# Kernel tuning notes

Hardware: AMD Instinct MI355X
Metric: run time of the kernel (lower is better)

Reference implementation:

```python
import jax, jax.numpy as jnp
import numpy as np
from jax import lax


def setup_inputs() -> dict:
    key = jax.random.key(0)
    k1, k2, k3 = jax.random.split(key, 3)
    x = jax.random.normal(k1, (16, 32, 48, 48, 48), dtype=jnp.float32)
    w = jax.random.normal(k2, (64, 32, 3, 3, 3), dtype=jnp.float32) * 0.05
    b = jax.random.normal(k3, (64,), dtype=jnp.float32) * 0.05
    return {"x": x, "w": w, "b": b}


def reference(x, w, b):
    # conv3d, stride=1, padding=1 (NCDHW / OIDHW)
    y = lax.conv_general_dilated(
        x, w,
        window_strides=(1, 1, 1),
        padding=[(1, 1), (1, 1), (1, 1)],
        dimension_numbers=("NCDHW", "OIDHW", "NCDHW"),
    )
    y = y + b[None, :, None, None, None]  # [N, Cout, 48, 48, 48]
    # maxpool3d kernel=2 stride=2 (ceil_mode=False)
    y = lax.reduce_window(
        y, -jnp.inf, lax.max,
        window_dimensions=(1, 1, 2, 2, 2),
        window_strides=(1, 1, 2, 2, 2),
        padding="VALID",
    )  # [N, Cout, 24, 24, 24]
    # logsumexp over channel dim (keepdim), then ReLU
    lse = jax.nn.logsumexp(y, axis=1, keepdims=True)  # [N, 1, 24, 24, 24]
    return jnp.maximum(lse, 0.0)
```

## Files before the change

kernel.cpp:

```cpp
#include <hip/hip_runtime.h>
#include <math.h>

#define CIN 32
#define COUT 64
#define DIM 48
#define PD 24
#define D3 110592

#define XP_POS 125000
#define XB_BYTES 128000000ull

typedef __bf16 bf16x8 __attribute__((ext_vector_type(8)));
typedef __bf16 bf16x4 __attribute__((ext_vector_type(4)));
typedef float f32x4 __attribute__((ext_vector_type(4)));

__device__ __forceinline__ unsigned bf16_rne(float f) {
    unsigned u = __builtin_bit_cast(unsigned, f);
    return (u + 0x7fffu + ((u >> 16) & 1u)) >> 16;
}

__global__ __launch_bounds__(256) void wpack_kernel(const float* __restrict__ w,
                                                    unsigned short* __restrict__ wg) {
    int i = blockIdx.x * 256 + threadIdx.x;
    if (i >= 27 * 64 * 32) return;
    int cin = i & 31, cout = (i >> 5) & 63, tap = i >> 11;
    float v = w[(cout * CIN + cin) * 27 + tap];
    wg[i] = (unsigned short)bf16_rne(v);
}

__global__ __launch_bounds__(256) void xpack_kernel(const float* __restrict__ x,
                                                    unsigned short* __restrict__ xb) {
    int i = blockIdx.x * 256 + threadIdx.x;
    if (i >= 16 * XP_POS) return;
    int pw = i % 50, t = i / 50, ph = t % 50, t2 = t / 50, pd = t2 % 50, n = t2 / 50;
    uint4* dst = (uint4*)(xb + (size_t)i * 32);
    int gd = pd - 1, gh = ph - 1, gw = pw - 1;
    if ((unsigned)gd < 48u && (unsigned)gh < 48u && (unsigned)gw < 48u) {
        const float* p = x + (size_t)n * CIN * D3 + ((size_t)gd * DIM + gh) * DIM + gw;
        unsigned pk[16];
#pragma unroll
        for (int cp = 0; cp < 16; ++cp) {
            float a = p[(size_t)(2 * cp) * D3];
            float b = p[(size_t)(2 * cp + 1) * D3];
            pk[cp] = bf16_rne(a) | (bf16_rne(b) << 16);
        }
#pragma unroll
        for (int q = 0; q < 4; ++q)
            dst[q] = make_uint4(pk[4 * q], pk[4 * q + 1], pk[4 * q + 2], pk[4 * q + 3]);
    } else {
        uint4 z = make_uint4(0, 0, 0, 0);
#pragma unroll
        for (int q = 0; q < 4; ++q) dst[q] = z;
    }
}

__global__ __launch_bounds__(256, 2) void conv_mfma_kernel(
    const unsigned short* __restrict__ xb, const unsigned short* __restrict__ wg,
    const float* __restrict__ bias, float* __restrict__ out)
{
    __shared__ __align__(16) unsigned short xs[1080 * 36];

    const int tid = threadIdx.x;
    const int bw = blockIdx.x % 3;
    const int bh = (blockIdx.x / 3) % 12;
    const int bd = (blockIdx.x / 36) % 6;
    const int n  = blockIdx.x / 216;

    const unsigned short* xtile = xb + (size_t)n * (XP_POS * 32)
                                + (size_t)(bd * 8) * (2500 * 32)
                                + (bh * 4) * (50 * 32) + (bw * 16) * 32;

    uint4 stg[17];
#pragma unroll
    for (int it = 0; it < 17; ++it) {
        int q = tid + it * 256;
        if (q < 4320) {
            int row = q >> 2, c = q & 3;
            int lw = row % 18, t = row / 18, lh = t % 6, ld = t / 6;
            stg[it] = *(const uint4*)(xtile + (size_t)ld * 80000 + lh * 1600 + lw * 32 + c * 8);
        }
    }
#pragma unroll
    for (int it = 0; it < 17; ++it) {
        int q = tid + it * 256;
        if (q < 4320) {
            int row = q >> 2, c = q & 3;
            char* p = (char*)xs + row * 72 + c * 16;
            *(uint2*)p       = make_uint2(stg[it].x, stg[it].y);
            *(uint2*)(p + 8) = make_uint2(stg[it].z, stg[it].w);
        }
    }

    const int lane = tid & 63;
    const int wv = tid >> 6;
    const int m  = lane & 15;
    const int ch = lane >> 4;

    const unsigned short* wgp = wg + m * 32 + ch * 8;

    float breg[4];
#pragma unroll
    for (int nt = 0; nt < 4; ++nt) breg[nt] = bias[nt * 16 + m];

    bf16x8 bcur[4], bnxt[4];
#pragma unroll
    for (int nt = 0; nt < 4; ++nt)
        bcur[nt] = *(const bf16x8*)(wgp + nt * 512);

    __syncthreads();

    f32x4 acc[2][4][4];
#pragma unroll
    for (int j = 0; j < 2; ++j)
#pragma unroll
        for (int i = 0; i < 4; ++i)
#pragma unroll
            for (int k = 0; k < 4; ++k)
                acc[j][i][k] = (f32x4)0.f;

#pragma unroll
    for (int tap = 0; tap < 27; ++tap) {
        if (tap < 26) {
#pragma unroll
            for (int nt = 0; nt < 4; ++nt)
                bnxt[nt] = *(const bf16x8*)(wgp + (tap + 1) * 2048 + nt * 512);
        }
        const int kd = tap / 9, kh = (tap / 3) % 3, kw = tap % 3;
        bf16x8 af[2][4];
#pragma unroll
        for (int j = 0; j < 2; ++j)
#pragma unroll
            for (int hz = 0; hz < 4; ++hz) {
                const int row = ((2 * wv + j + kd) * 6 + (hz + kh)) * 18 + (m + kw);
                const unsigned short* p = xs + row * 36 + ch * 8;
                bf16x4 lo = *(const bf16x4*)p;
                bf16x4 hi = *(const bf16x4*)(p + 4);
                af[j][hz] = __builtin_shufflevector(lo, hi, 0, 1, 2, 3, 4, 5, 6, 7);
            }
#pragma unroll
        for (int j = 0; j < 2; ++j)
#pragma unroll
            for (int hz = 0; hz < 4; ++hz)
#pragma unroll
                for (int nt = 0; nt < 4; ++nt)
                    acc[j][hz][nt] = __builtin_amdgcn_mfma_f32_16x16x32_bf16(
                        af[j][hz], bcur[nt], acc[j][hz][nt], 0, 0, 0);
#pragma unroll
        for (int nt = 0; nt < 4; ++nt) bcur[nt] = bnxt[nt];
    }
    __syncthreads();

    float* pooled = (float*)xs;
#pragma unroll
    for (int ph = 0; ph < 2; ++ph)
#pragma unroll
        for (int b = 0; b < 2; ++b)
#pragma unroll
            for (int nt = 0; nt < 4; ++nt) {
                float v =          acc[0][2 * ph][nt][2 * b];
                v = fmaxf(v,       acc[0][2 * ph][nt][2 * b + 1]);
                v = fmaxf(v,       acc[0][2 * ph + 1][nt][2 * b]);
                v = fmaxf(v,       acc[0][2 * ph + 1][nt][2 * b + 1]);
                v = fmaxf(v,       acc[1][2 * ph][nt][2 * b]);
                v = fmaxf(v,       acc[1][2 * ph][nt][2 * b + 1]);
                v = fmaxf(v,       acc[1][2 * ph + 1][nt][2 * b]);
                v = fmaxf(v,       acc[1][2 * ph + 1][nt][2 * b + 1]);
                int cell = (wv * 2 + ph) * 8 + 2 * ch + b;
                pooled[cell * 65 + nt * 16 + m] = v + breg[nt];
            }
    __syncthreads();

    if (tid < 64) {
        float mx = -INFINITY;
        for (int c = 0; c < 64; ++c) mx = fmaxf(mx, pooled[tid * 65 + c]);
        float s = 0.f;
        for (int c = 0; c < 64; ++c) s += __expf(pooled[tid * 65 + c] - mx);
        float r = fmaxf(mx + __logf(s), 0.f);
        int od = bd * 4 + (tid >> 4), oh = bh * 2 + ((tid >> 3) & 1), ow = bw * 8 + (tid & 7);
        out[((size_t)(n * PD + od) * PD + oh) * PD + ow] = r;
    }
}

__global__ __launch_bounds__(256, 3) void conv_mfma_r3(
    const float* __restrict__ x, const unsigned short* __restrict__ wg,
    const float* __restrict__ bias, float* __restrict__ out)
{
    __shared__ __align__(16) unsigned short xsr[648 * 40];
    const int tid = threadIdx.x;
    const int bw = blockIdx.x % 3;
    const int bh = (blockIdx.x / 3) % 12;
    const int bd = (blockIdx.x / 36) % 12;
    const int n  = blockIdx.x / 432;
    const int d0 = bd * 4 - 1, h0 = bh * 4 - 1, w0 = bw * 16 - 1;
    const float* xn = x + (size_t)n * CIN * D3;
    {
        const int cp = tid >> 4, sl = tid & 15;
        const float* xp0 = xn + (size_t)(cp * 2) * D3;
        for (int itb = 0; itb < 6; ++itb) {
            float f0[8], f1[8];
            int sv[8];
#pragma unroll
            for (int u = 0; u < 8; ++u) {
                const int s = sl + ((itb * 8 + u) << 4);
                sv[u] = s; f0[u] = 0.f; f1[u] = 0.f;
                if (s < 648) {
                    const int lw = s % 18, t = s / 18, lh = t % 6, ld = t / 6;
                    const int gd = d0 + ld, gh = h0 + lh, gw = w0 + lw;
                    if ((unsigned)gd < 48u && (unsigned)gh < 48u && (unsigned)gw < 48u) {
                        const float* p = xp0 + (gd * DIM + gh) * DIM + gw;
                        f0[u] = p[0]; f1[u] = p[D3];
                    }
                }
            }
#pragma unroll
            for (int u = 0; u < 8; ++u)
                if (sv[u] < 648)
                    ((unsigned*)xsr)[sv[u] * 20 + cp] = bf16_rne(f0[u]) | (bf16_rne(f1[u]) << 16);
        }
    }
    const int lane = tid & 63;
    const int wv = tid >> 6;
    const int m  = lane & 15;
    const int ch = lane >> 4;
    const unsigned short* wgp = wg + m * 32 + ch * 8;
    bf16x8 bcur[4], bnxt[4];
#pragma unroll
    for (int nt = 0; nt < 4; ++nt) bcur[nt] = *(const bf16x8*)(wgp + nt * 512);
    __syncthreads();
    f32x4 acc[4][4];
#pragma unroll
    for (int i = 0; i < 4; ++i)
#pragma unroll
        for (int j = 0; j < 4; ++j) acc[i][j] = (f32x4)0.f;
#pragma unroll
    for (int tap = 0; tap < 27; ++tap) {
        if (tap < 26) {
#pragma unroll
            for (int nt = 0; nt < 4; ++nt)
                bnxt[nt] = *(const bf16x8*)(wgp + (tap + 1) * 2048 + nt * 512);
        }
        const int kd = tap / 9, kh = (tap / 3) % 3, kw = tap % 3;
        bf16x8 af[4];
#pragma unroll
        for (int hz = 0; hz < 4; ++hz) {
            const int row = ((wv + kd) * 6 + (hz + kh)) * 18 + (m + kw);
            af[hz] = *(const bf16x8*)(xsr + row * 40 + ch * 8);
        }
#pragma unroll
        for (int hz = 0; hz < 4; ++hz)
#pragma unroll
            for (int nt = 0; nt < 4; ++nt)
                acc[hz][nt] = __builtin_amdgcn_mfma_f32_16x16x32_bf16(af[hz], bcur[nt], acc[hz][nt], 0, 0, 0);
#pragma unroll
        for (int nt = 0; nt < 4; ++nt) bcur[nt] = bnxt[nt];
    }
    __syncthreads();
    float* pmax = (float*)xsr;
#pragma unroll
    for (int ph = 0; ph < 2; ++ph)
#pragma unroll
        for (int b = 0; b < 2; ++b)
#pragma unroll
            for (int nt = 0; nt < 4; ++nt) {
                float v = fmaxf(fmaxf(acc[2 * ph][nt][2 * b], acc[2 * ph][nt][2 * b + 1]),
                                fmaxf(acc[2 * ph + 1][nt][2 * b], acc[2 * ph + 1][nt][2 * b + 1]));
                int pw = 2 * ch + b;
                pmax[((wv * 2 + ph) * 8 + pw) * 64 + nt * 16 + m] = v;
            }
    __syncthreads();
    float* pooled = pmax + 4096;
    for (int v = tid; v < 2048; v += 256) {
        int c = v & 63, cell = v >> 6;
        int pd = cell >> 4, ph = (cell >> 3) & 1, pw = cell & 7;
        int i1 = ((4 * pd + ph) * 8 + pw) * 64 + c;
        pooled[cell * 65 + c] = fmaxf(pmax[i1], pmax[i1 + 1024]) + bias[c];
    }
    __syncthreads();
    if (tid < 32) {
        int pd = tid >> 4, ph = (tid >> 3) & 1, pw = tid & 7;
        float mx = -INFINITY;
        for (int c = 0; c < 64; ++c) mx = fmaxf(mx, pooled[tid * 65 + c]);
        float s = 0.f;
        for (int c = 0; c < 64; ++c) s += __expf(pooled[tid * 65 + c] - mx);
        float r = fmaxf(mx + __logf(s), 0.f);
        int od = bd * 2 + pd, oh = bh * 2 + ph, ow = bw * 8 + pw;
        out[((size_t)(n * PD + od) * PD + oh) * PD + ow] = r;
    }
}

__global__ __launch_bounds__(256) void conv_fused_fallback(
    const float* __restrict__ x, const float* __restrict__ wsrc,
    const float* __restrict__ bias, float* __restrict__ out)
{
    __shared__ float smem[CIN * 216];
    const int tid = threadIdx.x;
    const int bid = blockIdx.x;
    const int tw = bid % 12, th = (bid / 12) % 12, td = (bid / 144) % 12, n = bid / 1728;
    const int d0 = td * 4, h0 = th * 4, w0 = tw * 4;
    const float* xn = x + (size_t)n * CIN * D3;
    for (int i = tid; i < CIN * 216; i += 256) {
        int cin = i / 216, r = i % 216;
        int dz = r / 36, hz = (r / 6) % 6, wz = r % 6;
        int gd = d0 - 1 + dz, gh = h0 - 1 + hz, gw = w0 - 1 + wz;
        float v = 0.f;
        if ((unsigned)gd < 48u && (unsigned)gh < 48u && (unsigned)gw < 48u)
            v = xn[((cin * DIM + gd) * DIM + gh) * DIM + gw];
        smem[i] = v;
    }
    __syncthreads();
    const int lane = tid & 63;
    const int wv = __builtin_amdgcn_readfirstlane(tid >> 6);
    const int cout0 = wv * 16;
    const int ld = lane >> 4, lh = (lane >> 2) & 3, lw = lane & 3;
    float acc[16];
#pragma unroll
    for (int c = 0; c < 16; ++c) acc[c] = 0.f;
    for (int cin = 0; cin < CIN; ++cin) {
        const int xb2 = cin * 216 + ld * 36 + lh * 6 + lw;
#pragma unroll
        for (int kd = 0; kd < 3; ++kd)
#pragma unroll
            for (int kh = 0; kh < 3; ++kh)
#pragma unroll
                for (int kw = 0; kw < 3; ++kw) {
                    const float xv = smem[xb2 + kd * 36 + kh * 6 + kw];
                    const int tap = (kd * 3 + kh) * 3 + kw;
#pragma unroll
                    for (int c = 0; c < 16; ++c)
                        acc[c] = fmaf(xv, wsrc[((cout0 + c) * CIN + cin) * 27 + tap], acc[c]);
                }
    }
    __syncthreads();
    float* cb = smem;
#pragma unroll
    for (int c = 0; c < 16; ++c) cb[(wv * 64 + lane) * 16 + c] = acc[c];
    __syncthreads();
    float* pool = smem + 4096;
    for (int v = tid; v < 512; v += 256) {
        const int pp = v >> 6, c = v & 63;
        const int pd = pp >> 2, ph = (pp >> 1) & 1, pw = pp & 1;
        float mv = -INFINITY;
#pragma unroll
        for (int i = 0; i < 2; ++i)
#pragma unroll
            for (int j = 0; j < 2; ++j)
#pragma unroll
                for (int k = 0; k < 2; ++k) {
                    const int l = ((2 * pd + i) << 4) | ((2 * ph + j) << 2) | (2 * pw + k);
                    mv = fmaxf(mv, cb[((c >> 4) * 64 + l) * 16 + (c & 15)]);
                }
        pool[pp * 64 + c] = mv + bias[c];
    }
    __syncthreads();
    if (tid < 8) {
        float mx = -INFINITY;
        for (int c = 0; c < 64; ++c) mx = fmaxf(mx, pool[tid * 64 + c]);
        float s = 0.f;
        for (int c = 0; c < 64; ++c) s += __expf(pool[tid * 64 + c] - mx);
        float r = fmaxf(mx + logf(s), 0.f);
        const int pd = tid >> 2, ph = (tid >> 1) & 1, pw = tid & 1;
        const int dp = td * 2 + pd, hp = th * 2 + ph, wp = tw * 2 + pw;
        out[(((size_t)n * PD + dp) * PD + hp) * PD + wp] = r;
    }
}

extern "C" void kernel_launch(void* const* d_in, const int* in_sizes, int n_in,
                              void* d_out, int out_size, void* d_ws, size_t ws_size,
                              hipStream_t stream) {
    const float* x = (const float*)d_in[0];
    const float* w = (const float*)d_in[1];
    const float* b = (const float*)d_in[2];
    float* out = (float*)d_out;

    const size_t wg_bytes = (size_t)(27 * 64 * 32) * sizeof(unsigned short);
    if (ws_size >= XB_BYTES + wg_bytes) {
        unsigned short* xbuf = (unsigned short*)d_ws;
        unsigned short* wgb  = (unsigned short*)((char*)d_ws + XB_BYTES);
        xpack_kernel<<<(16 * XP_POS + 255) / 256, 256, 0, stream>>>(x, xbuf);
        wpack_kernel<<<216, 256, 0, stream>>>(w, wgb);
        conv_mfma_kernel<<<16 * 6 * 12 * 3, 256, 0, stream>>>(xbuf, wgb, b, out);
    } else if (ws_size >= wg_bytes) {
        unsigned short* wgb = (unsigned short*)d_ws;
        wpack_kernel<<<216, 256, 0, stream>>>(w, wgb);
        conv_mfma_r3<<<16 * 12 * 12 * 3, 256, 0, stream>>>(x, wgb, b, out);
    } else {
        conv_fused_fallback<<<16 * 12 * 12 * 12, 256, 0, stream>>>(x, w, b, out);
    }
}
```

Before: 475.5 us.

## Split input packing into border-zero and LDS-transposed slice kernels; deepen weight prefetch

The fp32-to-bf16 channel-last packing is split into two kernels. One zeroes only the padding border. The other reads full W rows as float4 vectors, transposes through LDS, and writes 64-byte channel vectors. This replaces the strided per-element global reads of the old pack kernel, which touched 32 channel planes with scalar loads, with coalesced reads. Separately, the conv kernel's weight register prefetch becomes a three-slot ring two taps ahead, which hides load latency better at the cost of more VGPRs and an extra kernel launch.

New measurement: 502.7 us. +5.7%, slower.

```diff
diff --git a/kernel.cpp b/kernel.cpp
--- a/kernel.cpp
+++ b/kernel.cpp
@@ -28,29 +28,63 @@
     wg[i] = (unsigned short)bf16_rne(v);
 }
 
-__global__ __launch_bounds__(256) void xpack_kernel(const float* __restrict__ x,
-                                                    unsigned short* __restrict__ xb) {
+__global__ __launch_bounds__(256) void xborder_kernel(unsigned short* __restrict__ xb) {
     int i = blockIdx.x * 256 + threadIdx.x;
     if (i >= 16 * XP_POS) return;
-    int pw = i % 50, t = i / 50, ph = t % 50, t2 = t / 50, pd = t2 % 50, n = t2 / 50;
+    int pw = i % 50, t = i / 50, ph = t % 50, pd = (t / 50) % 50;
+    if ((unsigned)(pd - 1) < 48u && (unsigned)(ph - 1) < 48u && (unsigned)(pw - 1) < 48u)
+        return;
     uint4* dst = (uint4*)(xb + (size_t)i * 32);
-    int gd = pd - 1, gh = ph - 1, gw = pw - 1;
-    if ((unsigned)gd < 48u && (unsigned)gh < 48u && (unsigned)gw < 48u) {
-        const float* p = x + (size_t)n * CIN * D3 + ((size_t)gd * DIM + gh) * DIM + gw;
-        unsigned pk[16];
-#pragma unroll
-        for (int cp = 0; cp < 16; ++cp) {
-            float a = p[(size_t)(2 * cp) * D3];
-            float b = p[(size_t)(2 * cp + 1) * D3];
-            pk[cp] = bf16_rne(a) | (bf16_rne(b) << 16);
-        }
-#pragma unroll
-        for (int q = 0; q < 4; ++q)
-            dst[q] = make_uint4(pk[4 * q], pk[4 * q + 1], pk[4 * q + 2], pk[4 * q + 3]);
-    } else {
-        uint4 z = make_uint4(0, 0, 0, 0);
-#pragma unroll
-        for (int q = 0; q < 4; ++q) dst[q] = z;
+    uint4 z = make_uint4(0, 0, 0, 0);
+#pragma unroll
+    for (int q = 0; q < 4; ++q) dst[q] = z;
+}
+
+__global__ __launch_bounds__(256) void xslice_kernel(const float* __restrict__ x,
+                                                     unsigned short* __restrict__ xb) {
+    __shared__ unsigned lds32[768 * 17];
+
+    const int hc = blockIdx.x % 3;
+    const int gd = (blockIdx.x / 3) % 48;
+    const int n  = blockIdx.x / 144;
+    const int tid = threadIdx.x;
+
+    {
+        const int cp = tid >> 4, part = tid & 15;
+        const int ph = hc * 16 + part;
+        const float* src0 = x + ((size_t)(n * CIN + 2 * cp) * DIM + gd) * (DIM * DIM) + ph * DIM;
+        const float* src1 = src0 + D3;
+        float4 r0[12], r1[12];
+#pragma unroll
+        for (int k = 0; k < 12; ++k) r0[k] = *(const float4*)(src0 + 4 * k);
+#pragma unroll
+        for (int k = 0; k < 12; ++k) r1[k] = *(const float4*)(src1 + 4 * k);
+#pragma unroll
+        for (int k = 0; k < 12; ++k) {
+            const float a[4] = {r0[k].x, r0[k].y, r0[k].z, r0[k].w};
+            const float b[4] = {r1[k].x, r1[k].y, r1[k].z, r1[k].w};
+#pragma unroll
+            for (int j = 0; j < 4; ++j) {
+                int w = 4 * k + j;
+                lds32[(part * 48 + w) * 17 + cp] = bf16_rne(a[j]) | (bf16_rne(b[j]) << 16);
+            }
+        }
+    }
+    __syncthreads();
+
+    {
+        const int part = tid >> 4, tri = tid & 15;
+        const int ph = hc * 16 + part;
+        unsigned short* drow = xb + ((size_t)((n * 50 + gd + 1) * 50 + ph + 1) * 50 + 1) * 32;
+#pragma unroll
+        for (int j = 0; j < 3; ++j) {
+            const int w = 3 * tri + j;
+            const unsigned* s = &lds32[(part * 48 + w) * 17];
+            uint4* dst = (uint4*)(drow + (size_t)w * 32);
+#pragma unroll
+            for (int q = 0; q < 4; ++q)
+                dst[q] = make_uint4(s[4 * q], s[4 * q + 1], s[4 * q + 2], s[4 * q + 3]);
+        }
     }
 }
 
@@ -102,10 +136,12 @@
 #pragma unroll
     for (int nt = 0; nt < 4; ++nt) breg[nt] = bias[nt * 16 + m];
 
-    bf16x8 bcur[4], bnxt[4];
-#pragma unroll
-    for (int nt = 0; nt < 4; ++nt)
-        bcur[nt] = *(const bf16x8*)(wgp + nt * 512);
+    bf16x8 bq[3][4];
+#pragma unroll
+    for (int nt = 0; nt < 4; ++nt) {
+        bq[0][nt] = *(const bf16x8*)(wgp + nt * 512);
+        bq[1][nt] = *(const bf16x8*)(wgp + 2048 + nt * 512);
+    }
 
     __syncthreads();
 
@@ -120,10 +156,10 @@
 
 #pragma unroll
     for (int tap = 0; tap < 27; ++tap) {
-        if (tap < 26) {
+        if (tap < 25) {
 #pragma unroll
             for (int nt = 0; nt < 4; ++nt)
-                bnxt[nt] = *(const bf16x8*)(wgp + (tap + 1) * 2048 + nt * 512);
+                bq[(tap + 2) % 3][nt] = *(const bf16x8*)(wgp + (tap + 2) * 2048 + nt * 512);
         }
         const int kd = tap / 9, kh = (tap / 3) % 3, kw = tap % 3;
         bf16x8 af[2][4];
@@ -144,9 +180,7 @@
 #pragma unroll
                 for (int nt = 0; nt < 4; ++nt)
                     acc[j][hz][nt] = __builtin_amdgcn_mfma_f32_16x16x32_bf16(
-                        af[j][hz], bcur[nt], acc[j][hz][nt], 0, 0, 0);
-#pragma unroll
-        for (int nt = 0; nt < 4; ++nt) bcur[nt] = bnxt[nt];
+                        af[j][hz], bq[tap % 3][nt], acc[j][hz][nt], 0, 0, 0);
     }
     __syncthreads();
 
@@ -376,7 +410,8 @@
     if (ws_size >= XB_BYTES + wg_bytes) {
         unsigned short* xbuf = (unsigned short*)d_ws;
         unsigned short* wgb  = (unsigned short*)((char*)d_ws + XB_BYTES);
-        xpack_kernel<<<(16 * XP_POS + 255) / 256, 256, 0, stream>>>(x, xbuf);
+        xborder_kernel<<<(16 * XP_POS + 255) / 256, 256, 0, stream>>>(xbuf);
+        xslice_kernel<<<16 * 48 * 3, 256, 0, stream>>>(x, xbuf);
         wpack_kernel<<<216, 256, 0, stream>>>(w, wgb);
         conv_mfma_kernel<<<16 * 6 * 12 * 3, 256, 0, stream>>>(xbuf, wgb, b, out);
     } else if (ws_size >= wg_bytes) {
```
